# Performance work log

Hardware: AMD Instinct MI355X
Metric: run time of the kernel (lower is better)

The kernel has to match this reference:

```python
import jax, jax.numpy as jnp
import numpy as np

D, H, W = 20, 18, 18      # f_dim = (20, 72//4, 72//4); depth == feature_ch
PI = 3.14159              # constant used in the torch module


def make_grid():
    # matches make_coordinate_grid_3d: normalized coords in [-1, 1]
    x = 2.0 * jnp.arange(W, dtype=jnp.float32) / (W - 1) - 1.0
    y = 2.0 * jnp.arange(H, dtype=jnp.float32) / (H - 1) - 1.0
    z = 2.0 * jnp.arange(D, dtype=jnp.float32) / (D - 1) - 1.0
    xx = jnp.broadcast_to(x[None, None, :], (D, H, W))
    yy = jnp.broadcast_to(y[None, :, None], (D, H, W))
    zz = jnp.broadcast_to(z[:, None, None], (D, H, W))
    grid_xy = jnp.stack([xx, yy], axis=-1)   # (D,H,W,2), order (x, y)
    return grid_xy, zz


def trilinear_sample(vol, grid):
    # vol: (D,H,W); grid: (D,H,W,3) with (x,y,z) in [-1,1]
    # F.grid_sample defaults: mode='bilinear' (trilinear), padding='zeros', align_corners=False
    ix = ((grid[..., 0] + 1.0) * W - 1.0) * 0.5
    iy = ((grid[..., 1] + 1.0) * H - 1.0) * 0.5
    iz = ((grid[..., 2] + 1.0) * D - 1.0) * 0.5
    x0, y0, z0 = jnp.floor(ix), jnp.floor(iy), jnp.floor(iz)
    wx, wy, wz = ix - x0, iy - y0, iz - z0
    vflat = vol.reshape(-1)
    out = jnp.zeros_like(ix)
    for cz in (0, 1):
        for cy in (0, 1):
            for cx in (0, 1):
                xi = x0 + cx
                yi = y0 + cy
                zi = z0 + cz
                w = ((wx if cx else 1.0 - wx)
                     * (wy if cy else 1.0 - wy)
                     * (wz if cz else 1.0 - wz))
                valid = ((xi >= 0) & (xi < W) & (yi >= 0) & (yi < H)
                         & (zi >= 0) & (zi < D))
                xi_c = jnp.clip(xi, 0, W - 1).astype(jnp.int32)
                yi_c = jnp.clip(yi, 0, H - 1).astype(jnp.int32)
                zi_c = jnp.clip(zi, 0, D - 1).astype(jnp.int32)
                idx = (zi_c * H + yi_c) * W + xi_c
                out = out + jnp.where(valid, w * vflat[idx], 0.0)
    return out


def setup_inputs() -> dict:
    key = jax.random.key(0)
    ks = jax.random.split(key, 10)
    B, P, F = 4096, 256, 20
    s = 0.05
    return {
        "feature_map": jax.random.normal(ks[0], (B, F, H, W), jnp.float32),
        "para_code": jax.random.normal(ks[1], (B, P), jnp.float32),
        "W1": jax.random.normal(ks[2], (P, P), jnp.float32) * s,
        "b1": jax.random.normal(ks[3], (P,), jnp.float32) * s,
        "Ws": jax.random.normal(ks[4], (P, F), jnp.float32) * s,
        "bs": jax.random.normal(ks[5], (F,), jnp.float32) * s,
        "Wr": jax.random.normal(ks[6], (P, F), jnp.float32) * s,
        "br": jax.random.normal(ks[7], (F,), jnp.float32) * s,
        "Wt": jax.random.normal(ks[8], (P, 2 * F), jnp.float32) * s,
        "bt": jax.random.normal(ks[9], (2 * F,), jnp.float32) * s,
    }


def reference(feature_map, para_code, W1, b1, Ws, bs, Wr, br, Wt, bt):
    B, F = feature_map.shape[0], feature_map.shape[1]  # F == D == 20
    grid_xy, grid_z = make_grid()
    h = jax.nn.relu(para_code @ W1 + b1)                     # commn_linear
    scale = jax.nn.sigmoid(h @ Ws + bs) * 2.0                # (B,F)
    angle = jnp.tanh(h @ Wr + br) * PI                       # (B,F)
    trans = jnp.tanh(h @ Wt + bt).reshape(B, F, 2)           # (B,F,2)
    c, s = jnp.cos(angle), jnp.sin(angle)
    rot = jnp.stack([jnp.stack([c, -s], -1),
                     jnp.stack([s, c], -1)], -2)             # (B,F,2,2)
    g = grid_xy.reshape(F, H * W, 2)                          # depth == feature_ch
    # per-channel affine: rotate, scale, translate each grid point
    tg = jnp.einsum('bfij,fpj->bfpi', rot, g)                 # (B,F,HW,2)
    tg = tg * scale[:, :, None, None] + trans[:, :, None, :]
    full_grid = jnp.concatenate(
        [tg.reshape(B, F, H, W, 2),
         jnp.broadcast_to(grid_z, (B, F, H, W))[..., None]], axis=-1)
    return jax.vmap(trilinear_sample)(feature_map, full_grid)
```

## Files before the change

kernel.cpp:

```cpp
#include <hip/hip_runtime.h>

#define PI_F 3.14159f

__global__ __launch_bounds__(256) void params_kernel(
    const float* __restrict__ pc, const float* __restrict__ W1, const float* __restrict__ b1,
    const float* __restrict__ Ws, const float* __restrict__ bs,
    const float* __restrict__ Wr, const float* __restrict__ br,
    const float* __restrict__ Wt, const float* __restrict__ bt,
    float* __restrict__ params)
{
    __shared__ float hbuf[4][260];
    __shared__ float raw[4][80];

    const int t    = threadIdx.x;
    const int lane = t & 63;
    const int b0   = blockIdx.x * 4;

    float pval[4][4];
    #pragma unroll
    for (int g = 0; g < 4; ++g)
        #pragma unroll
        for (int c = 0; c < 4; ++c)
            pval[g][c] = pc[(size_t)(b0 + g) * 256 + c * 64 + lane];

    float acc[4];
    #pragma unroll
    for (int g = 0; g < 4; ++g) acc[g] = b1[t];

    #pragma unroll
    for (int c = 0; c < 4; ++c) {
        for (int kk = 0; kk < 64; ++kk) {
            float w = W1[(c * 64 + kk) * 256 + t];
            #pragma unroll
            for (int g = 0; g < 4; ++g) {
                float pk = __int_as_float(
                    __builtin_amdgcn_readlane(__float_as_int(pval[g][c]), kk));
                acc[g] = fmaf(pk, w, acc[g]);
            }
        }
    }
    #pragma unroll
    for (int g = 0; g < 4; ++g) hbuf[g][t] = fmaxf(acc[g], 0.0f);
    __syncthreads();

    for (int task = t; task < 320; task += 256) {
        int g   = task / 80;
        int col = task - g * 80;
        const float* Wcol;
        float bias;
        int stride;
        if (col < 20)      { Wcol = Ws + col;        bias = bs[col];      stride = 20; }
        else if (col < 40) { Wcol = Wr + (col - 20); bias = br[col - 20]; stride = 20; }
        else               { Wcol = Wt + (col - 40); bias = bt[col - 40]; stride = 40; }
        const float4* h4 = (const float4*)hbuf[g];
        float a = bias;
        for (int k4 = 0; k4 < 64; ++k4) {
            float4 h = h4[k4];
            int k = k4 * 4;
            a = fmaf(h.x, Wcol[k * stride], a);
            a = fmaf(h.y, Wcol[(k + 1) * stride], a);
            a = fmaf(h.z, Wcol[(k + 2) * stride], a);
            a = fmaf(h.w, Wcol[(k + 3) * stride], a);
        }
        raw[g][col] = a;
    }
    __syncthreads();

    for (int task = t; task < 80; task += 256) {
        int g = task / 20;
        int f = task - g * 20;
        float sc  = 2.0f / (1.0f + expf(-raw[g][f]));
        float ang = PI_F * tanhf(raw[g][20 + f]);
        float tx  = tanhf(raw[g][40 + 2 * f]);
        float ty  = tanhf(raw[g][40 + 2 * f + 1]);
        float c = cosf(ang), s = sinf(ang);
        float* o = params + ((size_t)(b0 + g) * 20 + f) * 8;
        o[0] = 9.0f * sc * c;  o[1] = -9.0f * sc * s;  o[2] = fmaf(9.0f, tx, 10.5f);
        o[3] = 9.0f * sc * s;  o[4] =  9.0f * sc * c;  o[5] = fmaf(9.0f, ty, 10.5f);
        o[6] = 0.0f;           o[7] = 0.0f;
    }
}

template<int D>
struct Stage {
    static constexpr int   Z0  = (D == 0) ? -1 : (40 * D - 19) / 38;
    static constexpr float W1v = (float)((40.0 * D - 19.0) / 38.0 - (double)Z0);
    static constexpr float W0v = 1.0f - W1v;
    static constexpr bool  V0  = (Z0 >= 0);
    static constexpr bool  V1  = (Z0 + 1 <= 19);

    static __device__ __forceinline__ void go(const float (&v)[20], float* vol, int w) {
        float I;
        if constexpr (V0 && V1)  I = fmaf(v[Z0], W0v, v[Z0 + 1] * W1v);
        else if constexpr (V0)   I = v[Z0] * W0v;
        else                     I = v[(Z0 + 1) < 0 ? 0 : (Z0 + 1)] * W1v;
        vol[D * 484 + w] = I;
        Stage<D + 1>::go(v, vol, w);
    }
};
template<> struct Stage<20> {
    static __device__ __forceinline__ void go(const float (&)[20], float*, int) {}
};

template<int D>
struct Run {
    static __device__ __forceinline__ void go(const float* __restrict__ pb,
                                              const float* vol,
                                              float X, float Y,
                                              float* __restrict__ ob) {
        float4 pA = *(const float4*)(pb + D * 8);
        float2 pB = *(const float2*)(pb + D * 8 + 4);

        float ix = fmaf(pA.x, X, fmaf(pA.y, Y, pA.z));
        float iy = fmaf(pA.w, X, fmaf(pB.x, Y, pB.y));

        float fx = floorf(ix), fy = floorf(iy);
        float u1 = ix - fx, v1 = iy - fy;
        float u0 = 1.0f - u1, v0 = 1.0f - v1;

        int xb = min(max((int)fx, 0), 20);
        int yb = min(max((int)fy, 0), 20);

        const float* s = vol + D * 484 + yb * 22 + xb;
        float t00 = s[0], t01 = s[1], t10 = s[22], t11 = s[23];

        float r = fmaf(fmaf(t01, u1, t00 * u0), v0,
                       fmaf(t11, u1, t10 * u0) * v1);
        ob[D * 324] = r;

        Run<D + 1>::go(pb, vol, X, Y, ob);
    }
};
template<> struct Run<20> {
    static __device__ __forceinline__ void go(const float*, const float*,
                                              float, float, float*) {}
};

__global__ __launch_bounds__(384) void sample_kernel(
    const float* __restrict__ fmap, const float* __restrict__ params,
    float* __restrict__ out)
{
    __shared__ __align__(16) float vol[20 * 484];

    const int b = blockIdx.x;
    const int t = threadIdx.x;

    float4* v4 = (float4*)vol;
    for (int i = t; i < 2420; i += 384) v4[i] = make_float4(0.f, 0.f, 0.f, 0.f);
    __syncthreads();

    int yy = 0, xx = 0;
    if (t < 324) {
        yy = t / 18;
        xx = t - yy * 18;
        const float* fb = fmap + (size_t)b * 6480;
        float v[20];
        #pragma unroll
        for (int dz = 0; dz < 20; ++dz) v[dz] = fb[dz * 324 + t];
        const int w = (yy + 2) * 22 + (xx + 2);
        Stage<0>::go(v, vol, w);
    }
    __syncthreads();

    if (t >= 324) return;

    const float X = xx * (2.0f / 17.0f) - 1.0f;
    const float Y = yy * (2.0f / 17.0f) - 1.0f;
    const float* pb = params + (size_t)b * 160;
    float* ob = out + (size_t)b * 6480 + t;

    Run<0>::go(pb, vol, X, Y, ob);
}

extern "C" void kernel_launch(void* const* d_in, const int* in_sizes, int n_in,
                              void* d_out, int out_size, void* d_ws, size_t ws_size,
                              hipStream_t stream)
{
    const float* fmap = (const float*)d_in[0];
    const float* pc   = (const float*)d_in[1];
    const float* W1   = (const float*)d_in[2];
    const float* b1   = (const float*)d_in[3];
    const float* Ws   = (const float*)d_in[4];
    const float* bs   = (const float*)d_in[5];
    const float* Wr   = (const float*)d_in[6];
    const float* br   = (const float*)d_in[7];
    const float* Wt   = (const float*)d_in[8];
    const float* bt   = (const float*)d_in[9];
    float* out    = (float*)d_out;
    float* params = (float*)d_ws;

    const int B = in_sizes[0] / (20 * 18 * 18);

    params_kernel<<<B / 4, 256, 0, stream>>>(pc, W1, b1, Ws, bs, Wr, br, Wt, bt, params);
    sample_kernel<<<B, 384, 0, stream>>>(fmap, params, out);
}
```

Baseline: 243.4 us.

## Shrink padded LDS volume to 20x20 with clamped coords and batch gathers

```diff
diff --git a/kernel.cpp b/kernel.cpp
--- a/kernel.cpp
+++ b/kernel.cpp
@@ -75,8 +75,8 @@
         float ty  = tanhf(raw[g][40 + 2 * f + 1]);
         float c = cosf(ang), s = sinf(ang);
         float* o = params + ((size_t)(b0 + g) * 20 + f) * 8;
-        o[0] = 9.0f * sc * c;  o[1] = -9.0f * sc * s;  o[2] = fmaf(9.0f, tx, 10.5f);
-        o[3] = 9.0f * sc * s;  o[4] =  9.0f * sc * c;  o[5] = fmaf(9.0f, ty, 10.5f);
+        o[0] = 9.0f * sc * c;  o[1] = -9.0f * sc * s;  o[2] = fmaf(9.0f, tx, 9.5f);
+        o[3] = 9.0f * sc * s;  o[4] =  9.0f * sc * c;  o[5] = fmaf(9.0f, ty, 9.5f);
         o[6] = 0.0f;           o[7] = 0.0f;
     }
 }
@@ -94,7 +94,7 @@
         if constexpr (V0 && V1)  I = fmaf(v[Z0], W0v, v[Z0 + 1] * W1v);
         else if constexpr (V0)   I = v[Z0] * W0v;
         else                     I = v[(Z0 + 1) < 0 ? 0 : (Z0 + 1)] * W1v;
-        vol[D * 484 + w] = I;
+        vol[D * 400 + w] = I;
         Stage<D + 1>::go(v, vol, w);
     }
 };
@@ -102,51 +102,17 @@
     static __device__ __forceinline__ void go(const float (&)[20], float*, int) {}
 };
 
-template<int D>
-struct Run {
-    static __device__ __forceinline__ void go(const float* __restrict__ pb,
-                                              const float* vol,
-                                              float X, float Y,
-                                              float* __restrict__ ob) {
-        float4 pA = *(const float4*)(pb + D * 8);
-        float2 pB = *(const float2*)(pb + D * 8 + 4);
-
-        float ix = fmaf(pA.x, X, fmaf(pA.y, Y, pA.z));
-        float iy = fmaf(pA.w, X, fmaf(pB.x, Y, pB.y));
-
-        float fx = floorf(ix), fy = floorf(iy);
-        float u1 = ix - fx, v1 = iy - fy;
-        float u0 = 1.0f - u1, v0 = 1.0f - v1;
-
-        int xb = min(max((int)fx, 0), 20);
-        int yb = min(max((int)fy, 0), 20);
-
-        const float* s = vol + D * 484 + yb * 22 + xb;
-        float t00 = s[0], t01 = s[1], t10 = s[22], t11 = s[23];
-
-        float r = fmaf(fmaf(t01, u1, t00 * u0), v0,
-                       fmaf(t11, u1, t10 * u0) * v1);
-        ob[D * 324] = r;
-
-        Run<D + 1>::go(pb, vol, X, Y, ob);
-    }
-};
-template<> struct Run<20> {
-    static __device__ __forceinline__ void go(const float*, const float*,
-                                              float, float, float*) {}
-};
-
-__global__ __launch_bounds__(384) void sample_kernel(
+__global__ __launch_bounds__(384, 8) void sample_kernel(
     const float* __restrict__ fmap, const float* __restrict__ params,
     float* __restrict__ out)
 {
-    __shared__ __align__(16) float vol[20 * 484];
+    __shared__ __align__(16) float vol[8024];
 
     const int b = blockIdx.x;
     const int t = threadIdx.x;
 
     float4* v4 = (float4*)vol;
-    for (int i = t; i < 2420; i += 384) v4[i] = make_float4(0.f, 0.f, 0.f, 0.f);
+    for (int i = t; i < 2006; i += 384) v4[i] = make_float4(0.f, 0.f, 0.f, 0.f);
     __syncthreads();
 
     int yy = 0, xx = 0;
@@ -157,7 +123,7 @@
         float v[20];
         #pragma unroll
         for (int dz = 0; dz < 20; ++dz) v[dz] = fb[dz * 324 + t];
-        const int w = (yy + 2) * 22 + (xx + 2);
+        const int w = (yy + 1) * 20 + (xx + 1);
         Stage<0>::go(v, vol, w);
     }
     __syncthreads();
@@ -169,7 +135,38 @@
     const float* pb = params + (size_t)b * 160;
     float* ob = out + (size_t)b * 6480 + t;
 
-    Run<0>::go(pb, vol, X, Y, ob);
+    #pragma unroll
+    for (int G = 0; G < 5; ++G) {
+        float u1[4], v1[4];
+        int base[4];
+        #pragma unroll
+        for (int j = 0; j < 4; ++j) {
+            const int D = G * 4 + j;
+            float4 pA = *(const float4*)(pb + D * 8);
+            float2 pB = *(const float2*)(pb + D * 8 + 4);
+            float ix = fmaf(pA.x, X, fmaf(pA.y, Y, pA.z));
+            float iy = fmaf(pA.w, X, fmaf(pB.x, Y, pB.y));
+            ix = fminf(fmaxf(ix, 0.0f), 19.0f);
+            iy = fminf(fmaxf(iy, 0.0f), 19.0f);
+            float fx = floorf(ix), fy = floorf(iy);
+            u1[j] = ix - fx;
+            v1[j] = iy - fy;
+            base[j] = D * 400 + (int)fy * 20 + (int)fx;
+        }
+        float t00[4], t01[4], t10[4], t11[4];
+        #pragma unroll
+        for (int j = 0; j < 4; ++j) {
+            const float* s = vol + base[j];
+            t00[j] = s[0]; t01[j] = s[1]; t10[j] = s[20]; t11[j] = s[21];
+        }
+        #pragma unroll
+        for (int j = 0; j < 4; ++j) {
+            float u0 = 1.0f - u1[j], v0 = 1.0f - v1[j];
+            float r = fmaf(fmaf(t01[j], u1[j], t00[j] * u0), v0,
+                           fmaf(t11[j], u1[j], t10[j] * u0) * v1[j]);
+            ob[(G * 4 + j) * 324] = r;
+        }
+    }
 }
 
 extern "C" void kernel_launch(void* const* d_in, const int* in_sizes, int n_in,
```

Result: no change. 246.6 us (+1.3%).
